# Optimization experiments

Hardware: AMD Instinct MI355X
Metric: run time of the kernel (lower is better)

## Reference

```python
import jax, jax.numpy as jnp
import numpy as np

N_BITS = 8
OUTLIER_THRESHOLD = 3.0  # in units of per-token std
QMAX = 2.0 ** (N_BITS - 1) - 1.0  # 127 for int8
EPS = 1e-6


def setup_inputs() -> dict:
    key = jax.random.key(0)
    kx, kw, kb = jax.random.split(key, 3)
    B, S, D_in, D_out = 4, 4096, 2048, 2048
    x = jax.random.normal(kx, (B, S, D_in), dtype=jnp.float32)
    # nn.Linear default init scale ~ 1/sqrt(in_features)
    W = jax.random.normal(kw, (D_out, D_in), dtype=jnp.float32) / np.sqrt(D_in)
    b = jax.random.normal(kb, (D_out,), dtype=jnp.float32) / np.sqrt(D_in)
    return {"x": x, "W": W, "b": b}


def _dynamic_outlier_quant(y):
    # Per-token (last-dim) dynamic quantization with outlier awareness:
    #   1) outliers = values with |y| > threshold * std(token)
    #   2) inliers are fake-quantized to int8 with per-token absmax scale
    #      computed over the clamped (inlier) range
    #   3) outliers are kept at full precision
    std = jnp.std(y, axis=-1, keepdims=True)            # [B, S, 1]
    thr = OUTLIER_THRESHOLD * std
    outlier_mask = jnp.abs(y) > thr                      # [B, S, D]
    y_clamped = jnp.clip(y, -thr, thr)
    scale = jnp.max(jnp.abs(y_clamped), axis=-1, keepdims=True) / QMAX
    scale = jnp.maximum(scale, EPS)
    y_q = jnp.round(y_clamped / scale) * scale           # fake-quant inliers
    return jnp.where(outlier_mask, y, y_q)


def reference(x, W, b):
    # Linear: y = x @ W^T + b  -> [B, S, D_out]
    y = jnp.einsum("bsd,od->bso", x, W) + b
    return _dynamic_outlier_quant(y)
```

## Files before the change

### kernel.cpp

```cpp
#include <hip/hip_runtime.h>
#include <hip/hip_bf16.h>


typedef __attribute__((ext_vector_type(8))) short bf16x8;
typedef __attribute__((ext_vector_type(4))) float f32x4;
typedef __attribute__((ext_vector_type(8))) unsigned short u16x8;

#define QMAX_F 127.0f
#define THR_SIG 3.0f
#define EPS_F 1e-6f

__device__ __forceinline__ unsigned short f2bf(float f) {
    unsigned int u = __builtin_bit_cast(unsigned int, f);
    unsigned int r = u + 0x7fffu + ((u >> 16) & 1u);
    return (unsigned short)(r >> 16);
}

__device__ __forceinline__ void gl_lds16(const unsigned short* g, unsigned short* l) {
    __builtin_amdgcn_global_load_lds((const __attribute__((address_space(1))) void*)g,
                                     (__attribute__((address_space(3))) void*)l, 16, 0, 0);
}

__global__ __launch_bounds__(256) void k_convert(const float* __restrict__ in,
                                                 unsigned short* __restrict__ out,
                                                 long long n) {
    long long i = ((long long)blockIdx.x * 256 + threadIdx.x) * 8;
    if (i + 8 <= n) {
        f32x4 a = *(const f32x4*)(in + i);
        f32x4 b = *(const f32x4*)(in + i + 4);
        u16x8 o;
#pragma unroll
        for (int j = 0; j < 4; ++j) { o[j] = f2bf(a[j]); o[4 + j] = f2bf(b[j]); }
        *(u16x8*)(out + i) = o;
    }
}

#define STGA(h, i, tt)                                                              \
    gl_lds16(aSrc + (size_t)((h) * 128 + (i) * 64) * K + (tt) * 64,                 \
             &lds[((tt) & 1) * 32768 + (h) * 8192 + (i) * 4096 + dstW])
#define STGB(h, i, tt)                                                              \
    gl_lds16(bSrc + (size_t)((h) * 128 + (i) * 64) * K + (tt) * 64,                 \
             &lds[((tt) & 1) * 32768 + 16384 + (h) * 8192 + (i) * 4096 + dstW])

__global__ __launch_bounds__(512, 2) void k_gemm8(const unsigned short* __restrict__ A,
                                                  const unsigned short* __restrict__ B,
                                                  const float* __restrict__ bias,
                                                  float* __restrict__ C,
                                                  int M, int N, int K) {
    __shared__ unsigned short lds[65536];

    const int nbn = N >> 8;
    const int nwg = gridDim.x;
    int lin = blockIdx.x;
    int swz = lin;
    if ((nwg & 7) == 0) {
        int cpx = nwg >> 3;
        swz = (lin & 7) * cpx + (lin >> 3);
    }
    const int bm = swz / nbn, bn = swz % nbn;
    const int rowBase = bm << 8, colBase = bn << 8;

    const int tid = threadIdx.x;
    const int lane = tid & 63, w = tid >> 6;
    const int wr = w >> 2, wc = w & 3;

    const int lrow = lane >> 3;
    const int lslot = (lane & 7) ^ lrow;
    const unsigned short* aSrc = A + (size_t)(rowBase + w * 8 + lrow) * K + lslot * 8;
    const unsigned short* bSrc = B + (size_t)(colBase + w * 8 + lrow) * K + lslot * 8;
    const int dstW = w * 512;

    const int fr = lane & 15;
    const int ps0 = (((lane >> 4) ^ (lane & 7))) * 8;
    const int aO0 = wr * 8192 + fr * 64 + ps0;
    const int aO1 = wr * 8192 + fr * 64 + (ps0 ^ 32);
    const int bO0 = (wc >> 1) * 8192 + ((wc & 1) * 64 + fr) * 64 + ps0;
    const int bO1 = (wc >> 1) * 8192 + ((wc & 1) * 64 + fr) * 64 + (ps0 ^ 32);

    f32x4 acc[8][4];
#pragma unroll
    for (int i = 0; i < 8; ++i)
#pragma unroll
        for (int j = 0; j < 4; ++j) acc[i][j] = (f32x4){0.f, 0.f, 0.f, 0.f};

    const int nt = K >> 6;

    STGA(0, 0, 0); STGA(0, 1, 0); STGA(1, 0, 0); STGA(1, 1, 0);
    STGB(0, 0, 0); STGB(0, 1, 0); STGB(1, 0, 0); STGB(1, 1, 0);
    STGB(0, 0, 1); STGB(0, 1, 1); STGB(1, 0, 1); STGB(1, 1, 1);
    asm volatile("s_waitcnt vmcnt(4)" ::: "memory");
    __builtin_amdgcn_sched_barrier(0);
    __builtin_amdgcn_s_barrier();

    for (int t = 0; t < nt; ++t) {
        const unsigned short* Ab = lds + (t & 1) * 32768;
        const unsigned short* Bb = Ab + 16384;
        bf16x8 aQ[8], bLo[4], bHi[4];

#pragma unroll
        for (int mi = 0; mi < 4; ++mi) {
            aQ[2 * mi] = *(const bf16x8*)(Ab + aO0 + mi * 1024);
            aQ[2 * mi + 1] = *(const bf16x8*)(Ab + aO1 + mi * 1024);
        }
#pragma unroll
        for (int ni = 0; ni < 2; ++ni) {
            bLo[2 * ni] = *(const bf16x8*)(Bb + bO0 + ni * 1024);
            bLo[2 * ni + 1] = *(const bf16x8*)(Bb + bO1 + ni * 1024);
        }
        if (t + 1 < nt) { STGA(0, 0, t + 1); STGA(0, 1, t + 1); }
        __builtin_amdgcn_s_barrier();
        __builtin_amdgcn_s_setprio(1);
#pragma unroll
        for (int mi = 0; mi < 4; ++mi)
#pragma unroll
            for (int ni = 0; ni < 2; ++ni) {
                acc[mi][ni] = __builtin_amdgcn_mfma_f32_16x16x32_bf16(
                    aQ[2 * mi], bLo[2 * ni], acc[mi][ni], 0, 0, 0);
                acc[mi][ni] = __builtin_amdgcn_mfma_f32_16x16x32_bf16(
                    aQ[2 * mi + 1], bLo[2 * ni + 1], acc[mi][ni], 0, 0, 0);
            }
        __builtin_amdgcn_s_setprio(0);
        __builtin_amdgcn_sched_barrier(0);
        __builtin_amdgcn_s_barrier();

#pragma unroll
        for (int ni = 0; ni < 2; ++ni) {
            bHi[2 * ni] = *(const bf16x8*)(Bb + bO0 + (ni + 2) * 1024);
            bHi[2 * ni + 1] = *(const bf16x8*)(Bb + bO1 + (ni + 2) * 1024);
        }
        if (t + 1 < nt) { STGA(1, 0, t + 1); STGA(1, 1, t + 1); }
        __builtin_amdgcn_s_barrier();
        __builtin_amdgcn_s_setprio(1);
#pragma unroll
        for (int mi = 0; mi < 4; ++mi)
#pragma unroll
            for (int ni = 0; ni < 2; ++ni) {
                acc[mi][2 + ni] = __builtin_amdgcn_mfma_f32_16x16x32_bf16(
                    aQ[2 * mi], bHi[2 * ni], acc[mi][2 + ni], 0, 0, 0);
                acc[mi][2 + ni] = __builtin_amdgcn_mfma_f32_16x16x32_bf16(
                    aQ[2 * mi + 1], bHi[2 * ni + 1], acc[mi][2 + ni], 0, 0, 0);
            }
        __builtin_amdgcn_s_setprio(0);
        __builtin_amdgcn_sched_barrier(0);
        __builtin_amdgcn_s_barrier();

#pragma unroll
        for (int mi = 0; mi < 4; ++mi) {
            aQ[2 * mi] = *(const bf16x8*)(Ab + aO0 + (mi + 4) * 1024);
            aQ[2 * mi + 1] = *(const bf16x8*)(Ab + aO1 + (mi + 4) * 1024);
        }
        if (t + 2 < nt) { STGB(0, 0, t + 2); STGB(0, 1, t + 2); }
        __builtin_amdgcn_s_barrier();
        __builtin_amdgcn_s_setprio(1);
#pragma unroll
        for (int mi = 0; mi < 4; ++mi)
#pragma unroll
            for (int ni = 0; ni < 2; ++ni) {
                acc[4 + mi][2 + ni] = __builtin_amdgcn_mfma_f32_16x16x32_bf16(
                    aQ[2 * mi], bHi[2 * ni], acc[4 + mi][2 + ni], 0, 0, 0);
                acc[4 + mi][2 + ni] = __builtin_amdgcn_mfma_f32_16x16x32_bf16(
                    aQ[2 * mi + 1], bHi[2 * ni + 1], acc[4 + mi][2 + ni], 0, 0, 0);
            }
        __builtin_amdgcn_s_setprio(0);
        __builtin_amdgcn_sched_barrier(0);
        __builtin_amdgcn_s_barrier();

        if (t + 2 < nt) { STGB(1, 0, t + 2); STGB(1, 1, t + 2); }
        __builtin_amdgcn_s_barrier();
        __builtin_amdgcn_s_setprio(1);
#pragma unroll
        for (int mi = 0; mi < 4; ++mi)
#pragma unroll
            for (int ni = 0; ni < 2; ++ni) {
                acc[4 + mi][ni] = __builtin_amdgcn_mfma_f32_16x16x32_bf16(
                    aQ[2 * mi], bLo[2 * ni], acc[4 + mi][ni], 0, 0, 0);
                acc[4 + mi][ni] = __builtin_amdgcn_mfma_f32_16x16x32_bf16(
                    aQ[2 * mi + 1], bLo[2 * ni + 1], acc[4 + mi][ni], 0, 0, 0);
            }
        __builtin_amdgcn_s_setprio(0);
        __builtin_amdgcn_sched_barrier(0);
        if (t < nt - 2) {
            asm volatile("s_waitcnt vmcnt(4)" ::: "memory");
        } else {
            asm volatile("s_waitcnt vmcnt(0)" ::: "memory");
        }
        __builtin_amdgcn_sched_barrier(0);
        __builtin_amdgcn_s_barrier();
    }

    const int rowoff = (lane >> 4) * 4;
#pragma unroll
    for (int ni = 0; ni < 4; ++ni) {
        int gc = colBase + wc * 64 + ni * 16 + fr;
        float bv = bias[gc];
#pragma unroll
        for (int mi = 0; mi < 8; ++mi) {
            int gr = rowBase + wr * 128 + mi * 16 + rowoff;
#pragma unroll
            for (int r = 0; r < 4; ++r)
                C[(size_t)(gr + r) * N + gc] = acc[mi][ni][r] + bv;
        }
    }
}

__global__ __launch_bounds__(256) void k_gemm_f32(const float* __restrict__ Av,
                                                  const float* __restrict__ Bv,
                                                  const float* __restrict__ bias,
                                                  float* __restrict__ C,
                                                  int M, int N, int K) {
    __shared__ unsigned short sA[128 * 40];
    __shared__ unsigned short sB[128 * 40];

    const int nbn = N / 128;
    const int nwg = gridDim.x;
    int lin = blockIdx.x;
    int swz = lin;
    if ((nwg & 7) == 0) {
        int cpx = nwg >> 3;
        swz = (lin & 7) * cpx + (lin >> 3);
    }
    const int bm = swz / nbn, bn = swz % nbn;
    const int rowBase = bm * 128, colBase = bn * 128;

    const int tid = threadIdx.x;
    const int lane = tid & 63, wave = tid >> 6;
    const int wr = wave >> 1, wc = wave & 1;
    const int fr = lane & 15;
    const int kblk = (lane >> 4) * 8;

    f32x4 acc[4][4];
#pragma unroll
    for (int i = 0; i < 4; ++i)
#pragma unroll
        for (int j = 0; j < 4; ++j) acc[i][j] = (f32x4){0.f, 0.f, 0.f, 0.f};

    const int nk = K / 32;
    for (int kt = 0; kt < nk; ++kt) {
        const int kb = kt * 32;
        __syncthreads();
#pragma unroll
        for (int cc = 0; cc < 2; ++cc) {
            int c = tid + cc * 256;
            int row = c >> 2;
            int k8 = (c & 3) * 8;
            const float* gA = Av + (size_t)(rowBase + row) * K + kb + k8;
            const float* gB = Bv + (size_t)(colBase + row) * K + kb + k8;
            f32x4 a0 = *(const f32x4*)gA, a1 = *(const f32x4*)(gA + 4);
            f32x4 b0 = *(const f32x4*)gB, b1 = *(const f32x4*)(gB + 4);
            u16x8 va, vb;
#pragma unroll
            for (int j = 0; j < 4; ++j) {
                va[j] = f2bf(a0[j]); va[4 + j] = f2bf(a1[j]);
                vb[j] = f2bf(b0[j]); vb[4 + j] = f2bf(b1[j]);
            }
            *(u16x8*)&sA[row * 40 + k8] = va;
            *(u16x8*)&sB[row * 40 + k8] = vb;
        }
        __syncthreads();

        bf16x8 af[4], bfrag[4];
#pragma unroll
        for (int mi = 0; mi < 4; ++mi)
            af[mi] = *(const bf16x8*)&sA[(wr * 64 + mi * 16 + fr) * 40 + kblk];
#pragma unroll
        for (int ni = 0; ni < 4; ++ni)
            bfrag[ni] = *(const bf16x8*)&sB[(wc * 64 + ni * 16 + fr) * 40 + kblk];
#pragma unroll
        for (int mi = 0; mi < 4; ++mi)
#pragma unroll
            for (int ni = 0; ni < 4; ++ni)
                acc[mi][ni] = __builtin_amdgcn_mfma_f32_16x16x32_bf16(
                    af[mi], bfrag[ni], acc[mi][ni], 0, 0, 0);
    }

    const int rowoff = (lane >> 4) * 4;
#pragma unroll
    for (int ni = 0; ni < 4; ++ni) {
        int gc = colBase + wc * 64 + ni * 16 + fr;
        float bv = bias[gc];
#pragma unroll
        for (int mi = 0; mi < 4; ++mi) {
            int gr = rowBase + wr * 64 + mi * 16 + rowoff;
#pragma unroll
            for (int r = 0; r < 4; ++r)
                C[(size_t)(gr + r) * N + gc] = acc[mi][ni][r] + bv;
        }
    }
}

__global__ __launch_bounds__(256) void k_quant(float* __restrict__ y, int D) {
    float* p = y + (size_t)blockIdx.x * D;
    const int tid = threadIdx.x;
    f32x4 v0 = *(const f32x4*)(p + tid * 8);
    f32x4 v1 = *(const f32x4*)(p + tid * 8 + 4);

    float s = 0.f, ss = 0.f;
#pragma unroll
    for (int j = 0; j < 4; ++j) {
        s += v0[j] + v1[j];
        ss += v0[j] * v0[j] + v1[j] * v1[j];
    }
#pragma unroll
    for (int off = 32; off > 0; off >>= 1) {
        s += __shfl_down(s, off, 64);
        ss += __shfl_down(ss, off, 64);
    }

    __shared__ float rs[4], rss[4], bc[2];
    const int wave = tid >> 6, lane = tid & 63;
    if (lane == 0) { rs[wave] = s; rss[wave] = ss; }
    __syncthreads();
    if (tid == 0) {
        float S = rs[0] + rs[1] + rs[2] + rs[3];
        float SS = rss[0] + rss[1] + rss[2] + rss[3];
        float mean = S / (float)D;
        float var = fmaxf(SS / (float)D - mean * mean, 0.f);
        bc[0] = THR_SIG * sqrtf(var);
    }
    __syncthreads();
    const float thr = bc[0];

    float m = 0.f;
#pragma unroll
    for (int j = 0; j < 4; ++j) {
        m = fmaxf(m, fminf(fabsf(v0[j]), thr));
        m = fmaxf(m, fminf(fabsf(v1[j]), thr));
    }
#pragma unroll
    for (int off = 32; off > 0; off >>= 1) m = fmaxf(m, __shfl_down(m, off, 64));
    if (lane == 0) rs[wave] = m;
    __syncthreads();
    if (tid == 0) {
        float mm = fmaxf(fmaxf(rs[0], rs[1]), fmaxf(rs[2], rs[3]));
        bc[1] = fmaxf(mm / QMAX_F, EPS_F);
    }
    __syncthreads();
    const float scale = bc[1];

#pragma unroll
    for (int j = 0; j < 4; ++j) {
        {
            float v = v0[j];
            float c = fminf(fmaxf(v, -thr), thr);
            float q = rintf(c / scale) * scale;
            v0[j] = (fabsf(v) > thr) ? v : q;
        }
        {
            float v = v1[j];
            float c = fminf(fmaxf(v, -thr), thr);
            float q = rintf(c / scale) * scale;
            v1[j] = (fabsf(v) > thr) ? v : q;
        }
    }
    *(f32x4*)(p + tid * 8) = v0;
    *(f32x4*)(p + tid * 8 + 4) = v1;
}

extern "C" void kernel_launch(void* const* d_in, const int* in_sizes, int n_in,
                              void* d_out, int out_size, void* d_ws, size_t ws_size,
                              hipStream_t stream) {
    const float* x = (const float*)d_in[0];
    const float* W = (const float*)d_in[1];
    const float* b = (const float*)d_in[2];
    float* out = (float*)d_out;

    const int Dout = in_sizes[2];
    const int Din = in_sizes[1] / Dout;
    const int M = in_sizes[0] / Din;

    const size_t nA = (size_t)M * Din;
    const size_t nB = (size_t)Dout * Din;
    const size_t need = (nA + nB) * sizeof(unsigned short);
    const bool fits8 = (M % 256 == 0) && (Dout % 256 == 0) && (Din % 64 == 0) && (Din >= 256);
    const bool pre = (ws_size >= need) && fits8;

    if (pre) {
        unsigned short* xb = (unsigned short*)d_ws;
        unsigned short* wb = xb + nA;
        int gA = (int)((nA + 8 * 256 - 1) / (8 * 256));
        int gB = (int)((nB + 8 * 256 - 1) / (8 * 256));
        k_convert<<<gA, 256, 0, stream>>>(x, xb, (long long)nA);
        k_convert<<<gB, 256, 0, stream>>>(W, wb, (long long)nB);
        int gridGemm = (M / 256) * (Dout / 256);
        k_gemm8<<<gridGemm, 512, 0, stream>>>(xb, wb, b, out, M, Dout, Din);
    } else {
        int gridGemm = (M / 128) * (Dout / 128);
        k_gemm_f32<<<gridGemm, 256, 0, stream>>>(x, W, b, out, M, Dout, Din);
    }
    k_quant<<<M, 256, 0, stream>>>(out, Dout);
}
```

Before: 214.9 us.

## Switch GEMM to 4 waves each computing 128x128 sub-tiles

```diff
diff --git a/kernel.cpp b/kernel.cpp
--- a/kernel.cpp
+++ b/kernel.cpp
@@ -36,13 +36,13 @@
 }
 
 #define STGA(h, i, tt)                                                              \
-    gl_lds16(aSrc + (size_t)((h) * 128 + (i) * 64) * K + (tt) * 64,                 \
-             &lds[((tt) & 1) * 32768 + (h) * 8192 + (i) * 4096 + dstW])
+    gl_lds16(aSrc + (size_t)((h) * 128 + (i) * 32) * K + (tt) * 64,                 \
+             &lds[((tt) & 1) * 32768 + (h) * 8192 + (i) * 2048 + dstW])
 #define STGB(h, i, tt)                                                              \
-    gl_lds16(bSrc + (size_t)((h) * 128 + (i) * 64) * K + (tt) * 64,                 \
-             &lds[((tt) & 1) * 32768 + 16384 + (h) * 8192 + (i) * 4096 + dstW])
-
-__global__ __launch_bounds__(512, 2) void k_gemm8(const unsigned short* __restrict__ A,
+    gl_lds16(bSrc + (size_t)((h) * 128 + (i) * 32) * K + (tt) * 64,                 \
+             &lds[((tt) & 1) * 32768 + 16384 + (h) * 8192 + (i) * 2048 + dstW])
+
+__global__ __launch_bounds__(256, 1) void k_gemm4(const unsigned short* __restrict__ A,
                                                   const unsigned short* __restrict__ B,
                                                   const float* __restrict__ bias,
                                                   float* __restrict__ C,
@@ -62,7 +62,7 @@
 
     const int tid = threadIdx.x;
     const int lane = tid & 63, w = tid >> 6;
-    const int wr = w >> 2, wc = w & 3;
+    const int wr = w >> 1, wc = w & 1;
 
     const int lrow = lane >> 3;
     const int lslot = (lane & 7) ^ lrow;
@@ -74,113 +74,124 @@
     const int ps0 = (((lane >> 4) ^ (lane & 7))) * 8;
     const int aO0 = wr * 8192 + fr * 64 + ps0;
     const int aO1 = wr * 8192 + fr * 64 + (ps0 ^ 32);
-    const int bO0 = (wc >> 1) * 8192 + ((wc & 1) * 64 + fr) * 64 + ps0;
-    const int bO1 = (wc >> 1) * 8192 + ((wc & 1) * 64 + fr) * 64 + (ps0 ^ 32);
-
-    f32x4 acc[8][4];
+    const int bO0 = wc * 8192 + fr * 64 + ps0;
+    const int bO1 = wc * 8192 + fr * 64 + (ps0 ^ 32);
+
+    f32x4 acc[8][8];
 #pragma unroll
     for (int i = 0; i < 8; ++i)
 #pragma unroll
-        for (int j = 0; j < 4; ++j) acc[i][j] = (f32x4){0.f, 0.f, 0.f, 0.f};
+        for (int j = 0; j < 8; ++j) acc[i][j] = (f32x4){0.f, 0.f, 0.f, 0.f};
 
     const int nt = K >> 6;
 
-    STGA(0, 0, 0); STGA(0, 1, 0); STGA(1, 0, 0); STGA(1, 1, 0);
-    STGB(0, 0, 0); STGB(0, 1, 0); STGB(1, 0, 0); STGB(1, 1, 0);
-    STGB(0, 0, 1); STGB(0, 1, 1); STGB(1, 0, 1); STGB(1, 1, 1);
-    asm volatile("s_waitcnt vmcnt(4)" ::: "memory");
+#pragma unroll
+    for (int i = 0; i < 4; ++i) { STGA(0, i, 0); STGA(1, i, 0); }
+#pragma unroll
+    for (int i = 0; i < 4; ++i) { STGB(0, i, 0); STGB(1, i, 0); }
+#pragma unroll
+    for (int i = 0; i < 4; ++i) { STGB(0, i, 1); STGB(1, i, 1); }
+    asm volatile("s_waitcnt vmcnt(8)" ::: "memory");
     __builtin_amdgcn_sched_barrier(0);
     __builtin_amdgcn_s_barrier();
 
     for (int t = 0; t < nt; ++t) {
         const unsigned short* Ab = lds + (t & 1) * 32768;
         const unsigned short* Bb = Ab + 16384;
-        bf16x8 aQ[8], bLo[4], bHi[4];
+        bf16x8 aLo[8], aHi[8], bLo[8], bHi[8];
 
 #pragma unroll
         for (int mi = 0; mi < 4; ++mi) {
-            aQ[2 * mi] = *(const bf16x8*)(Ab + aO0 + mi * 1024);
-            aQ[2 * mi + 1] = *(const bf16x8*)(Ab + aO1 + mi * 1024);
-        }
-#pragma unroll
-        for (int ni = 0; ni < 2; ++ni) {
+            aLo[2 * mi] = *(const bf16x8*)(Ab + aO0 + mi * 1024);
+            aLo[2 * mi + 1] = *(const bf16x8*)(Ab + aO1 + mi * 1024);
+        }
+#pragma unroll
+        for (int ni = 0; ni < 4; ++ni) {
             bLo[2 * ni] = *(const bf16x8*)(Bb + bO0 + ni * 1024);
             bLo[2 * ni + 1] = *(const bf16x8*)(Bb + bO1 + ni * 1024);
         }
-        if (t + 1 < nt) { STGA(0, 0, t + 1); STGA(0, 1, t + 1); }
+        if (t + 1 < nt) {
+#pragma unroll
+            for (int i = 0; i < 4; ++i) STGA(0, i, t + 1);
+        }
         __builtin_amdgcn_s_barrier();
         __builtin_amdgcn_s_setprio(1);
 #pragma unroll
-        for (int mi = 0; mi < 4; ++mi)
-#pragma unroll
-            for (int ni = 0; ni < 2; ++ni) {
-                acc[mi][ni] = __builtin_amdgcn_mfma_f32_16x16x32_bf16(
-                    aQ[2 * mi], bLo[2 * ni], acc[mi][ni], 0, 0, 0);
-                acc[mi][ni] = __builtin_amdgcn_mfma_f32_16x16x32_bf16(
-                    aQ[2 * mi + 1], bLo[2 * ni + 1], acc[mi][ni], 0, 0, 0);
-            }
+        for (int ks = 0; ks < 2; ++ks)
+#pragma unroll
+            for (int mi = 0; mi < 4; ++mi)
+#pragma unroll
+                for (int ni = 0; ni < 4; ++ni)
+                    acc[mi][ni] = __builtin_amdgcn_mfma_f32_16x16x32_bf16(
+                        aLo[2 * mi + ks], bLo[2 * ni + ks], acc[mi][ni], 0, 0, 0);
         __builtin_amdgcn_s_setprio(0);
         __builtin_amdgcn_sched_barrier(0);
         __builtin_amdgcn_s_barrier();
 
 #pragma unroll
-        for (int ni = 0; ni < 2; ++ni) {
-            bHi[2 * ni] = *(const bf16x8*)(Bb + bO0 + (ni + 2) * 1024);
-            bHi[2 * ni + 1] = *(const bf16x8*)(Bb + bO1 + (ni + 2) * 1024);
-        }
-        if (t + 1 < nt) { STGA(1, 0, t + 1); STGA(1, 1, t + 1); }
+        for (int ni = 0; ni < 4; ++ni) {
+            bHi[2 * ni] = *(const bf16x8*)(Bb + bO0 + (ni + 4) * 1024);
+            bHi[2 * ni + 1] = *(const bf16x8*)(Bb + bO1 + (ni + 4) * 1024);
+        }
+        if (t + 1 < nt) {
+#pragma unroll
+            for (int i = 0; i < 4; ++i) STGA(1, i, t + 1);
+        }
         __builtin_amdgcn_s_barrier();
         __builtin_amdgcn_s_setprio(1);
 #pragma unroll
-        for (int mi = 0; mi < 4; ++mi)
-#pragma unroll
-            for (int ni = 0; ni < 2; ++ni) {
-                acc[mi][2 + ni] = __builtin_amdgcn_mfma_f32_16x16x32_bf16(
-                    aQ[2 * mi], bHi[2 * ni], acc[mi][2 + ni], 0, 0, 0);
-                acc[mi][2 + ni] = __builtin_amdgcn_mfma_f32_16x16x32_bf16(
-                    aQ[2 * mi + 1], bHi[2 * ni + 1], acc[mi][2 + ni], 0, 0, 0);
-            }
+        for (int ks = 0; ks < 2; ++ks)
+#pragma unroll
+            for (int mi = 0; mi < 4; ++mi)
+#pragma unroll
+                for (int ni = 0; ni < 4; ++ni)
+                    acc[mi][4 + ni] = __builtin_amdgcn_mfma_f32_16x16x32_bf16(
+                        aLo[2 * mi + ks], bHi[2 * ni + ks], acc[mi][4 + ni], 0, 0, 0);
         __builtin_amdgcn_s_setprio(0);
         __builtin_amdgcn_sched_barrier(0);
         __builtin_amdgcn_s_barrier();
 
 #pragma unroll
         for (int mi = 0; mi < 4; ++mi) {
-            aQ[2 * mi] = *(const bf16x8*)(Ab + aO0 + (mi + 4) * 1024);
-            aQ[2 * mi + 1] = *(const bf16x8*)(Ab + aO1 + (mi + 4) * 1024);
-        }
-        if (t + 2 < nt) { STGB(0, 0, t + 2); STGB(0, 1, t + 2); }
+            aHi[2 * mi] = *(const bf16x8*)(Ab + aO0 + (mi + 4) * 1024);
+            aHi[2 * mi + 1] = *(const bf16x8*)(Ab + aO1 + (mi + 4) * 1024);
+        }
+        if (t + 2 < nt) {
+#pragma unroll
+            for (int i = 0; i < 4; ++i) STGB(0, i, t + 2);
+        }
         __builtin_amdgcn_s_barrier();
         __builtin_amdgcn_s_setprio(1);
 #pragma unroll
-        for (int mi = 0; mi < 4; ++mi)
-#pragma unroll
-            for (int ni = 0; ni < 2; ++ni) {
-                acc[4 + mi][2 + ni] = __builtin_amdgcn_mfma_f32_16x16x32_bf16(
-                    aQ[2 * mi], bHi[2 * ni], acc[4 + mi][2 + ni], 0, 0, 0);
-                acc[4 + mi][2 + ni] = __builtin_amdgcn_mfma_f32_16x16x32_bf16(
-                    aQ[2 * mi + 1], bHi[2 * ni + 1], acc[4 + mi][2 + ni], 0, 0, 0);
-            }
+        for (int ks = 0; ks < 2; ++ks)
+#pragma unroll
+            for (int mi = 0; mi < 4; ++mi)
+#pragma unroll
+                for (int ni = 0; ni < 4; ++ni)
+                    acc[4 + mi][4 + ni] = __builtin_amdgcn_mfma_f32_16x16x32_bf16(
+                        aHi[2 * mi + ks], bHi[2 * ni + ks], acc[4 + mi][4 + ni], 0, 0, 0);
         __builtin_amdgcn_s_setprio(0);
         __builtin_amdgcn_sched_barrier(0);
         __builtin_amdgcn_s_barrier();
 
-        if (t + 2 < nt) { STGB(1, 0, t + 2); STGB(1, 1, t + 2); }
+        if (t + 2 < nt) {
+#pragma unroll
+            for (int i = 0; i < 4; ++i) STGB(1, i, t + 2);
+        }
         __builtin_amdgcn_s_barrier();
         __builtin_amdgcn_s_setprio(1);
 #pragma unroll
-        for (int mi = 0; mi < 4; ++mi)
-#pragma unroll
-            for (int ni = 0; ni < 2; ++ni) {
-                acc[4 + mi][ni] = __builtin_amdgcn_mfma_f32_16x16x32_bf16(
-                    aQ[2 * mi], bLo[2 * ni], acc[4 + mi][ni], 0, 0, 0);
-                acc[4 + mi][ni] = __builtin_amdgcn_mfma_f32_16x16x32_bf16(
-                    aQ[2 * mi + 1], bLo[2 * ni + 1], acc[4 + mi][ni], 0, 0, 0);
-            }
+        for (int ks = 0; ks < 2; ++ks)
+#pragma unroll
+            for (int mi = 0; mi < 4; ++mi)
+#pragma unroll
+                for (int ni = 0; ni < 4; ++ni)
+                    acc[4 + mi][ni] = __builtin_amdgcn_mfma_f32_16x16x32_bf16(
+                        aHi[2 * mi + ks], bLo[2 * ni + ks], acc[4 + mi][ni], 0, 0, 0);
         __builtin_amdgcn_s_setprio(0);
         __builtin_amdgcn_sched_barrier(0);
         if (t < nt - 2) {
-            asm volatile("s_waitcnt vmcnt(4)" ::: "memory");
+            asm volatile("s_waitcnt vmcnt(8)" ::: "memory");
         } else {
             asm volatile("s_waitcnt vmcnt(0)" ::: "memory");
         }
@@ -190,8 +201,8 @@
 
     const int rowoff = (lane >> 4) * 4;
 #pragma unroll
-    for (int ni = 0; ni < 4; ++ni) {
-        int gc = colBase + wc * 64 + ni * 16 + fr;
+    for (int ni = 0; ni < 8; ++ni) {
+        int gc = colBase + wc * 128 + ni * 16 + fr;
         float bv = bias[gc];
 #pragma unroll
         for (int mi = 0; mi < 8; ++mi) {
@@ -382,7 +393,7 @@
         k_convert<<<gA, 256, 0, stream>>>(x, xb, (long long)nA);
         k_convert<<<gB, 256, 0, stream>>>(W, wb, (long long)nB);
         int gridGemm = (M / 256) * (Dout / 256);
-        k_gemm8<<<gridGemm, 512, 0, stream>>>(xb, wb, b, out, M, Dout, Din);
+        k_gemm4<<<gridGemm, 256, 0, stream>>>(xb, wb, b, out, M, Dout, Din);
     } else {
         int gridGemm = (M / 128) * (Dout / 128);
         k_gemm_f32<<<gridGemm, 256, 0, stream>>>(x, W, b, out, M, Dout, Din);
```

Result: no change. 214.8 us (-0.0%).
